# Performance work log

Measured on AMD Instinct MI355X. Metric: run time of the kernel, lower is better.

The kernel has to match this reference:

```python
import jax, jax.numpy as jnp
import numpy as np

NHEAD = 8
DIM_HEAD = 64
SCALE = DIM_HEAD ** (-0.5)


def setup_inputs() -> dict:
    key = jax.random.key(0)
    k1, k2, k3 = jax.random.split(key, 3)
    B, C, X, Y = 16, 256, 64, 64
    x = jax.random.normal(k1, (B, C, X, Y), dtype=jnp.float32)
    # 1x1 conv weights, represented as [out_channels, in_channels]
    w_qkv = jax.random.normal(k2, (3 * NHEAD * DIM_HEAD, C), dtype=jnp.float32) * (C ** -0.5)
    w_out = jax.random.normal(k3, (C, NHEAD * DIM_HEAD), dtype=jnp.float32) * ((NHEAD * DIM_HEAD) ** -0.5)
    return {"x": x, "w_qkv": w_qkv, "w_out": w_out}


def reference(x, w_qkv, w_out):
    B, C, X, Y = x.shape
    h, d = NHEAD, DIM_HEAD
    n = X * Y
    # 1x1 conv == channel-wise matmul
    qkv = jnp.einsum('bcxy,oc->boxy', x, w_qkv)          # [B, 3*h*d, X, Y]
    qkv = qkv.reshape(B, 3, h, d, n)                     # chunk along channels then (h c)
    q, k, v = qkv[:, 0], qkv[:, 1], qkv[:, 2]            # each [B, h, d, n]
    q = jax.nn.softmax(q, axis=-2) * SCALE               # softmax over feature dim d
    k = jax.nn.softmax(k, axis=-1)                       # softmax over token dim n
    phi_kv = jnp.einsum('bhdn,bhen->bhde', k, v)         # [B, h, d, d]
    att = jnp.einsum('bhde,bhdn->bhen', phi_kv, q)       # [B, h, d, n]
    att = att.reshape(B, h * d, X, Y)
    out = jnp.einsum('bexy,ce->bcxy', att, w_out)        # [B, C, X, Y]
    return out
```

## Files before the change

kernel.cpp:

```cpp
#include <hip/hip_runtime.h>
#include <hip/hip_bf16.h>


typedef __attribute__((ext_vector_type(8))) short bf16x8;
typedef __attribute__((ext_vector_type(4))) float f32x4;

__device__ __forceinline__ unsigned short f2bf(float f) {
    union { float f; unsigned int i; } w; w.f = f;
    unsigned int r = w.i + 0x7FFFu + ((w.i >> 16) & 1u);
    return (unsigned short)(r >> 16);
}

__device__ __forceinline__ void gload16(const unsigned short* g, unsigned short* l) {
    __builtin_amdgcn_global_load_lds(
        (const __attribute__((address_space(1))) void*)(const void*)g,
        (__attribute__((address_space(3))) void*)(void*)l,
        16, 0, 0);
}

__global__ __launch_bounds__(256) void cvt_w_frag(
    const float* __restrict__ wqkv, unsigned short* __restrict__ wf)
{
    int g = blockIdx.x * 256 + threadIdx.x;
    int lane = g & 63;
    int ks   = (g >> 6) & 7;
    int w2   = (g >> 9) & 3;
    int h    = (g >> 11) & 7;
    int op   = g >> 14;
    int row = op * 512 + h * 64 + w2 * 16 + (lane & 15);
    int col = ks * 32 + (lane >> 4) * 8;
    const float* src = &wqkv[(size_t)row * 256 + col];
    float4 f0 = *(const float4*)&src[0];
    float4 f1 = *(const float4*)&src[4];
    unsigned short t[8] = {f2bf(f0.x), f2bf(f0.y), f2bf(f0.z), f2bf(f0.w),
                           f2bf(f1.x), f2bf(f1.y), f2bf(f1.z), f2bf(f1.w)};
    *(uint4*)&wf[(size_t)g * 8] = *(uint4*)t;
}

__global__ __launch_bounds__(256) void cvt_xT(
    const float* __restrict__ x, unsigned short* __restrict__ xT)
{
    const int nb = blockIdx.x * 64, cb = blockIdx.y * 64, b = blockIdx.z;
    __shared__ float Ts[64 * 65];
    const int tid = threadIdx.x;
    const int l = tid & 63, w = tid >> 6;
    const float* xb = x + ((size_t)b * 256 + cb) * 4096 + nb;
#pragma unroll
    for (int p = 0; p < 4; p++) {
        int c = p * 16 + (tid >> 4);
        int n4 = (tid & 15) * 4;
        float4 v = *(const float4*)&xb[(size_t)c * 4096 + n4];
        Ts[c * 65 + n4 + 0] = v.x; Ts[c * 65 + n4 + 1] = v.y;
        Ts[c * 65 + n4 + 2] = v.z; Ts[c * 65 + n4 + 3] = v.w;
    }
    __syncthreads();
    unsigned short t[16];
#pragma unroll
    for (int i = 0; i < 16; i++) t[i] = f2bf(Ts[(w * 16 + i) * 65 + l]);
    unsigned short* dst = xT + ((size_t)b * 4096 + nb + l) * 256 + cb + w * 16;
    *(uint4*)&dst[0] = *(uint4*)&t[0];
    *(uint4*)&dst[8] = *(uint4*)&t[8];
}

__global__ __launch_bounds__(256, 3) void q_gemm(
    const unsigned short* __restrict__ xT, const unsigned short* __restrict__ wf,
    unsigned short* __restrict__ qf)
{
    const int ch = blockIdx.x;
    const int h  = blockIdx.y;
    const int b  = blockIdx.z;
    const int tid  = threadIdx.x;
    const int lane = tid & 63;
    const int w    = tid >> 6;
    const int quad = lane >> 4;
    const int l15  = lane & 15;

    __shared__ unsigned short smem[16384];
    unsigned short* Bs = smem;
    float* red = (float*)smem;
    unsigned short* Qs = smem + 7168;

    const unsigned short* wfq = wf + ((size_t)((0 * 8 + h) * 4 + w) * 8) * 512 + lane * 8;
    bf16x8 aq[8];
#pragma unroll
    for (int i = 0; i < 8; i++) aq[i] = *(const bf16x8*)&wfq[i * 512];

    const int grow = lane >> 3;
    const int gch  = ((lane & 7) ^ grow) * 8;
    const int c0 = (quad ^ (l15 & 7)) * 8;
    const int c1 = ((quad + 4) ^ (l15 & 7)) * 8;

    for (int st = 0; st < 4; st++) {
        const int nb = ch * 512 + st * 128;
        const unsigned short* gbase =
            xT + ((size_t)b * 4096 + nb + w * 32 + grow) * 256 + gch;

        f32x4 accq[8];
#pragma unroll
        for (int i = 0; i < 8; i++) accq[i] = (f32x4)(0.f);

#pragma unroll
        for (int i = 0; i < 4; i++)
            gload16(gbase + i * 2048, Bs + w * 2048 + i * 512);
        __syncthreads();

#pragma unroll
        for (int ks = 0; ks < 4; ks++) {
            const int buf = ks & 1;
            if (ks < 3) {
                const unsigned short* gs = gbase + (ks + 1) * 64;
                unsigned short* ld = Bs + (buf ^ 1) * 8192 + w * 2048;
#pragma unroll
                for (int i = 0; i < 4; i++)
                    gload16(gs + i * 2048, ld + i * 512);
            }
            const unsigned short* bsr = Bs + buf * 8192 + l15 * 64;
#pragma unroll
            for (int nt = 0; nt < 8; nt++) {
                bf16x8 bv0 = *(const bf16x8*)&bsr[nt * 1024 + c0];
                bf16x8 bv1 = *(const bf16x8*)&bsr[nt * 1024 + c1];
                accq[nt] = __builtin_amdgcn_mfma_f32_16x16x32_bf16(aq[2 * ks], bv0, accq[nt], 0, 0, 0);
                accq[nt] = __builtin_amdgcn_mfma_f32_16x16x32_bf16(aq[2 * ks + 1], bv1, accq[nt], 0, 0, 0);
            }
            if (ks < 3) __syncthreads();
        }

#pragma unroll
        for (int nt = 0; nt < 8; nt++) {
#pragma unroll
            for (int r = 0; r < 4; r++) accq[nt][r] = __expf(accq[nt][r]);
            float s = accq[nt][0] + accq[nt][1] + accq[nt][2] + accq[nt][3];
            s += __shfl_xor(s, 16);
            s += __shfl_xor(s, 32);
            if (quad == 0) red[w * 128 + nt * 16 + l15] = s;
        }
        __syncthreads();
        if (tid < 128) {
            float t = red[tid] + red[128 + tid] + red[256 + tid] + red[384 + tid];
            red[512 + tid] = 0.125f / t;
        }
        __syncthreads();
#pragma unroll
        for (int nt = 0; nt < 8; nt++) {
            float li = red[512 + nt * 16 + l15];
            uint2 pp;
            pp.x = (unsigned int)f2bf(accq[nt][0] * li) |
                   ((unsigned int)f2bf(accq[nt][1] * li) << 16);
            pp.y = (unsigned int)f2bf(accq[nt][2] * li) |
                   ((unsigned int)f2bf(accq[nt][3] * li) << 16);
            *(uint2*)&Qs[(nt * 16 + l15) * 72 + w * 16 + quad * 4] = pp;
        }
        __syncthreads();
        {
            const int n = tid >> 1, half = tid & 1;
            const int nbIdx = ch * 4 + st;
            const int ksq = h * 2 + half;
            const size_t gbase2 =
                (((size_t)(b * 32 + nbIdx) * 16 + ksq) * 8 + (n >> 4)) * 64 + (n & 15);
#pragma unroll
            for (int u = 0; u < 4; u++)
                *(uint4*)&qf[(gbase2 + u * 16) * 8] = *(uint4*)&Qs[n * 72 + half * 32 + u * 8];
        }
        __syncthreads();
    }
}

__global__ __launch_bounds__(256, 2) void kv_phi(
    const unsigned short* __restrict__ xT, const unsigned short* __restrict__ wf,
    float* __restrict__ phi, float* __restrict__ lsum)
{
    const int ch = blockIdx.x;
    const int h  = blockIdx.y;
    const int b  = blockIdx.z;
    const int tid  = threadIdx.x;
    const int lane = tid & 63;
    const int w    = tid >> 6;
    const int quad = lane >> 4;
    const int l15  = lane & 15;

    __shared__ unsigned short smem[16384];
    unsigned short* Es = smem;
    unsigned short* Vs = smem + 8192;
    unsigned short* Bs = smem;

    const unsigned short* wfk = wf + ((size_t)((1 * 8 + h) * 4 + w) * 8) * 512 + lane * 8;
    const unsigned short* wfv = wf + ((size_t)((2 * 8 + h) * 4 + w) * 8) * 512 + lane * 8;

    f32x4 pacc[4];
#pragma unroll
    for (int i = 0; i < 4; i++) pacc[i] = (f32x4)(0.f);
    float lacc[4] = {0.f, 0.f, 0.f, 0.f};

    const int grow = lane >> 3;
    const int gch  = ((lane & 7) ^ grow) * 8;
    const int c0 = (quad ^ (l15 & 7)) * 8;
    const int c1 = ((quad + 4) ^ (l15 & 7)) * 8;

    for (int st = 0; st < 4; st++) {
        const int nb = ch * 512 + st * 128;
        const unsigned short* gbase =
            xT + ((size_t)b * 4096 + nb + w * 32 + grow) * 256 + gch;

        f32x4 acck[8], accv[8];
#pragma unroll
        for (int i = 0; i < 8; i++) {
            acck[i] = (f32x4)(0.f); accv[i] = (f32x4)(0.f);
        }

        __syncthreads();
#pragma unroll
        for (int i = 0; i < 4; i++)
            gload16(gbase + i * 2048, Bs + w * 2048 + i * 512);
        __syncthreads();

#pragma unroll
        for (int ks = 0; ks < 4; ks++) {
            const int buf = ks & 1;
            if (ks < 3) {
                const unsigned short* gs = gbase + (ks + 1) * 64;
                unsigned short* ld = Bs + (buf ^ 1) * 8192 + w * 2048;
#pragma unroll
                for (int i = 0; i < 4; i++)
                    gload16(gs + i * 2048, ld + i * 512);
            }
            bf16x8 ak0 = *(const bf16x8*)&wfk[(2 * ks) * 512];
            bf16x8 ak1 = *(const bf16x8*)&wfk[(2 * ks + 1) * 512];
            bf16x8 av0 = *(const bf16x8*)&wfv[(2 * ks) * 512];
            bf16x8 av1 = *(const bf16x8*)&wfv[(2 * ks + 1) * 512];
            const unsigned short* bsr = Bs + buf * 8192 + l15 * 64;
#pragma unroll
            for (int nt = 0; nt < 8; nt++) {
                bf16x8 bv0 = *(const bf16x8*)&bsr[nt * 1024 + c0];
                bf16x8 bv1 = *(const bf16x8*)&bsr[nt * 1024 + c1];
                acck[nt] = __builtin_amdgcn_mfma_f32_16x16x32_bf16(ak0, bv0, acck[nt], 0, 0, 0);
                accv[nt] = __builtin_amdgcn_mfma_f32_16x16x32_bf16(av0, bv0, accv[nt], 0, 0, 0);
                acck[nt] = __builtin_amdgcn_mfma_f32_16x16x32_bf16(ak1, bv1, acck[nt], 0, 0, 0);
                accv[nt] = __builtin_amdgcn_mfma_f32_16x16x32_bf16(av1, bv1, accv[nt], 0, 0, 0);
            }
            if (ks < 3) __syncthreads();
        }
        __syncthreads();

#pragma unroll
        for (int r = 0; r < 4; r++) {
            const int dl = quad * 4 + r;
            const int dbase = (w * 16 + dl) * 256 + (l15 & 7) * 2;
#pragma unroll
            for (int nt = 0; nt < 8; nt++) {
                const int pos = (2 * nt + (l15 >> 3)) ^ dl;
                float ek = __expf(acck[nt][r]);
                lacc[r] += ek;
                *(unsigned short*)((char*)Es + dbase + pos * 16) = f2bf(ek);
                *(unsigned short*)((char*)Vs + dbase + pos * 16) = f2bf(accv[nt][r]);
            }
        }
        __syncthreads();

#pragma unroll
        for (int k2 = 0; k2 < 4; k2++) {
            bf16x8 ae = *(bf16x8*)((char*)Es + (w * 16 + l15) * 256 +
                                   (((k2 * 4 + quad) ^ l15) * 16));
#pragma unroll
            for (int et = 0; et < 4; et++) {
                bf16x8 bv = *(bf16x8*)((char*)Vs + (et * 16 + l15) * 256 +
                                       (((k2 * 4 + quad) ^ l15) * 16));
                pacc[et] = __builtin_amdgcn_mfma_f32_16x16x32_bf16(ae, bv, pacc[et], 0, 0, 0);
            }
        }
    }

#pragma unroll
    for (int r = 0; r < 4; r++) {
        float s = lacc[r];
        s += __shfl_xor(s, 1); s += __shfl_xor(s, 2);
        s += __shfl_xor(s, 4); s += __shfl_xor(s, 8);
        if (l15 == 0)
            atomicAdd(&lsum[((size_t)b * 8 + h) * 64 + w * 16 + quad * 4 + r], s);
    }
    float* pp = phi + ((size_t)b * 8 + h) * 4096;
#pragma unroll
    for (int et = 0; et < 4; et++)
#pragma unroll
        for (int r = 0; r < 4; r++)
            atomicAdd(&pp[(w * 16 + quad * 4 + r) * 64 + et * 16 + l15], pacc[et][r]);
}

__global__ __launch_bounds__(256) void build_M(
    const float* __restrict__ phi, const float* __restrict__ lsum,
    const float* __restrict__ w_out, unsigned short* __restrict__ Mf)
{
    const int h = blockIdx.x, b = blockIdx.y;
    __shared__ float pT[64][68];
    const float* pp = phi + ((size_t)b * 8 + h) * 4096;
    const int tid = threadIdx.x;
    const int row = tid >> 2, ls = tid & 3;
#pragma unroll
    for (int u = 0; u < 4; u++) {
        int e0 = (ls + u * 4) * 4;
        float4 v = *(const float4*)&pp[row * 64 + e0];
        pT[e0 + 0][row] = v.x; pT[e0 + 1][row] = v.y;
        pT[e0 + 2][row] = v.z; pT[e0 + 3][row] = v.w;
    }
    __syncthreads();
    const int c = tid;
    float acc[64];
#pragma unroll
    for (int d = 0; d < 64; d++) acc[d] = 0.f;
    for (int e4 = 0; e4 < 16; e4++) {
        float4 wv = *(const float4*)&w_out[(size_t)c * 512 + h * 64 + e4 * 4];
        float wq[4] = {wv.x, wv.y, wv.z, wv.w};
#pragma unroll
        for (int qq = 0; qq < 4; qq++) {
            int e = e4 * 4 + qq;
#pragma unroll
            for (int d4 = 0; d4 < 16; d4++) {
                float4 p = *(const float4*)&pT[e][d4 * 4];
                acc[d4 * 4 + 0] += wq[qq] * p.x;
                acc[d4 * 4 + 1] += wq[qq] * p.y;
                acc[d4 * 4 + 2] += wq[qq] * p.z;
                acc[d4 * 4 + 3] += wq[qq] * p.w;
            }
        }
    }
    const float* lrow = lsum + ((size_t)b * 8 + h) * 64;
    unsigned short tmp[64];
#pragma unroll
    for (int d = 0; d < 64; d++) tmp[d] = f2bf(acc[d] / lrow[d]);
    const int ct = c >> 7, wr = (c >> 6) & 1, mi = (c >> 4) & 3, l15c = c & 15;
#pragma unroll
    for (int u = 0; u < 8; u++) {
        const int ksA = h * 2 + (u >> 2);
        const int quadA = u & 3;
        size_t gidx = ((((size_t)(b * 2 + ct) * 2 + wr) * 4 + mi) * 16 + ksA) * 64
                      + quadA * 16 + l15c;
        *(uint4*)&Mf[gidx * 8] = *(uint4*)&tmp[u * 8];
    }
}

__global__ __launch_bounds__(256, 3) void out_mfma(
    const unsigned short* __restrict__ Mf, const unsigned short* __restrict__ qf,
    float* __restrict__ out)
{
    const int nbIdx = blockIdx.x;
    const int ct    = blockIdx.y;
    const int b     = blockIdx.z;
    const int tid  = threadIdx.x;
    const int lane = tid & 63;
    const int w    = tid >> 6;
    const int wr   = w >> 1, wc = w & 1;
    const int quad = lane >> 4;
    const int l15  = lane & 15;

    f32x4 acc[4][4];
#pragma unroll
    for (int i = 0; i < 4; i++)
#pragma unroll
        for (int j = 0; j < 4; j++) acc[i][j] = (f32x4)(0.f);

    const unsigned short* Ab =
        Mf + ((((size_t)(b * 2 + ct) * 2 + wr) * 4) * 16) * 512 + lane * 8;
    const unsigned short* Bb =
        qf + (((size_t)(b * 32 + nbIdx) * 16) * 8) * 512 + lane * 8;

    for (int ks = 0; ks < 16; ks++) {
        bf16x8 af[4], bv[4];
#pragma unroll
        for (int mi = 0; mi < 4; mi++)
            af[mi] = *(const bf16x8*)&Ab[(size_t)(mi * 16 + ks) * 512];
#pragma unroll
        for (int ni = 0; ni < 4; ni++)
            bv[ni] = *(const bf16x8*)&Bb[(size_t)(ks * 8 + wc * 4 + ni) * 512];
#pragma unroll
        for (int mi = 0; mi < 4; mi++)
#pragma unroll
            for (int ni = 0; ni < 4; ni++)
                acc[mi][ni] = __builtin_amdgcn_mfma_f32_16x16x32_bf16(
                    af[mi], bv[ni], acc[mi][ni], 0, 0, 0);
    }
    float* ob = out + ((size_t)b * 256 + ct * 128 + wr * 64) * 4096
                + nbIdx * 128 + wc * 64;
#pragma unroll
    for (int mi = 0; mi < 4; mi++)
#pragma unroll
        for (int ni = 0; ni < 4; ni++)
#pragma unroll
            for (int r = 0; r < 4; r++)
                ob[(size_t)(mi * 16 + quad * 4 + r) * 4096 + ni * 16 + l15]
                    = acc[mi][ni][r];
}

extern "C" void kernel_launch(void* const* d_in, const int* in_sizes, int n_in,
                              void* d_out, int out_size, void* d_ws, size_t ws_size,
                              hipStream_t stream) {
    const float* x     = (const float*)d_in[0];
    const float* w_qkv = (const float*)d_in[1];
    const float* w_out = (const float*)d_in[2];
    float* out = (float*)d_out;

    char* ws = (char*)d_ws;
    unsigned short* qf = (unsigned short*)ws;
    unsigned short* wf = (unsigned short*)(ws + 67108864);
    float* lsum = (float*)(ws + 67895296);
    float* phi  = (float*)(ws + 67928064);
    unsigned short* Mf = (unsigned short*)(ws + 70025216);
    unsigned short* xT = (unsigned short*)(ws + 74219520);

    hipMemsetAsync(lsum, 0, (8192 + 524288) * sizeof(float), stream);

    cvt_w_frag<<<192, 256, 0, stream>>>(w_qkv, wf);
    cvt_xT<<<dim3(64, 4, 16), 256, 0, stream>>>(x, xT);
    q_gemm<<<dim3(8, 8, 16), 256, 0, stream>>>(xT, wf, qf);
    kv_phi<<<dim3(8, 8, 16), 256, 0, stream>>>(xT, wf, phi, lsum);
    build_M<<<dim3(8, 16), 256, 0, stream>>>(phi, lsum, w_out, Mf);
    out_mfma<<<dim3(32, 2, 16), 256, 0, stream>>>(Mf, qf, out);
}
```

Before: 262.9 us.

## Repartition kv_phi wave work by token rows instead of head-dim rows

Each wave in kv_phi now computes all 64 k/v feature rows for its own 32-token slice, instead of 16 feature rows across all 128 tokens. Each wave reads only its slice of the LDS activation tile and loads four weight fragments per k-step from global memory. This cuts LDS read traffic for the x tile but raises per-wave weight loads and register use for the fragment arrays and the 4x4 partial log-sum accumulators. The scatter into the exp/value staging buffers and the lsum atomics are re-indexed to match the new partition.

```diff
diff --git a/kernel.cpp b/kernel.cpp
--- a/kernel.cpp
+++ b/kernel.cpp
@@ -183,13 +183,17 @@
     unsigned short* Vs = smem + 8192;
     unsigned short* Bs = smem;
 
-    const unsigned short* wfk = wf + ((size_t)((1 * 8 + h) * 4 + w) * 8) * 512 + lane * 8;
-    const unsigned short* wfv = wf + ((size_t)((2 * 8 + h) * 4 + w) * 8) * 512 + lane * 8;
+    const unsigned short* wfkb = wf + ((size_t)(1 * 8 + h) * 4) * 8 * 512 + lane * 8;
+    const unsigned short* wfvb = wf + ((size_t)(2 * 8 + h) * 4) * 8 * 512 + lane * 8;
 
     f32x4 pacc[4];
 #pragma unroll
     for (int i = 0; i < 4; i++) pacc[i] = (f32x4)(0.f);
-    float lacc[4] = {0.f, 0.f, 0.f, 0.f};
+    float lacc[4][4];
+#pragma unroll
+    for (int i = 0; i < 4; i++)
+#pragma unroll
+        for (int j = 0; j < 4; j++) lacc[i][j] = 0.f;
 
     const int grow = lane >> 3;
     const int gch  = ((lane & 7) ^ grow) * 8;
@@ -201,11 +205,13 @@
         const unsigned short* gbase =
             xT + ((size_t)b * 4096 + nb + w * 32 + grow) * 256 + gch;
 
-        f32x4 acck[8], accv[8];
-#pragma unroll
-        for (int i = 0; i < 8; i++) {
-            acck[i] = (f32x4)(0.f); accv[i] = (f32x4)(0.f);
-        }
+        f32x4 acck[2][4], accv[2][4];
+#pragma unroll
+        for (int i = 0; i < 2; i++)
+#pragma unroll
+            for (int j = 0; j < 4; j++) {
+                acck[i][j] = (f32x4)(0.f); accv[i][j] = (f32x4)(0.f);
+            }
 
         __syncthreads();
 #pragma unroll
@@ -223,19 +229,26 @@
                 for (int i = 0; i < 4; i++)
                     gload16(gs + i * 2048, ld + i * 512);
             }
-            bf16x8 ak0 = *(const bf16x8*)&wfk[(2 * ks) * 512];
-            bf16x8 ak1 = *(const bf16x8*)&wfk[(2 * ks + 1) * 512];
-            bf16x8 av0 = *(const bf16x8*)&wfv[(2 * ks) * 512];
-            bf16x8 av1 = *(const bf16x8*)&wfv[(2 * ks + 1) * 512];
-            const unsigned short* bsr = Bs + buf * 8192 + l15 * 64;
-#pragma unroll
-            for (int nt = 0; nt < 8; nt++) {
-                bf16x8 bv0 = *(const bf16x8*)&bsr[nt * 1024 + c0];
-                bf16x8 bv1 = *(const bf16x8*)&bsr[nt * 1024 + c1];
-                acck[nt] = __builtin_amdgcn_mfma_f32_16x16x32_bf16(ak0, bv0, acck[nt], 0, 0, 0);
-                accv[nt] = __builtin_amdgcn_mfma_f32_16x16x32_bf16(av0, bv0, accv[nt], 0, 0, 0);
-                acck[nt] = __builtin_amdgcn_mfma_f32_16x16x32_bf16(ak1, bv1, acck[nt], 0, 0, 0);
-                accv[nt] = __builtin_amdgcn_mfma_f32_16x16x32_bf16(av1, bv1, accv[nt], 0, 0, 0);
+            const unsigned short* bsr = Bs + buf * 8192 + (w * 32 + l15) * 64;
+#pragma unroll
+            for (int s = 0; s < 2; s++) {
+                const int ks2 = 2 * ks + s;
+                const int cs = s ? c1 : c0;
+                bf16x8 ak[4], av[4];
+#pragma unroll
+                for (int dt = 0; dt < 4; dt++) {
+                    ak[dt] = *(const bf16x8*)&wfkb[(size_t)(dt * 8 + ks2) * 512];
+                    av[dt] = *(const bf16x8*)&wfvb[(size_t)(dt * 8 + ks2) * 512];
+                }
+                bf16x8 bv0 = *(const bf16x8*)&bsr[0 * 1024 + cs];
+                bf16x8 bv1 = *(const bf16x8*)&bsr[1 * 1024 + cs];
+#pragma unroll
+                for (int dt = 0; dt < 4; dt++) {
+                    acck[0][dt] = __builtin_amdgcn_mfma_f32_16x16x32_bf16(ak[dt], bv0, acck[0][dt], 0, 0, 0);
+                    accv[0][dt] = __builtin_amdgcn_mfma_f32_16x16x32_bf16(av[dt], bv0, accv[0][dt], 0, 0, 0);
+                    acck[1][dt] = __builtin_amdgcn_mfma_f32_16x16x32_bf16(ak[dt], bv1, acck[1][dt], 0, 0, 0);
+                    accv[1][dt] = __builtin_amdgcn_mfma_f32_16x16x32_bf16(av[dt], bv1, accv[1][dt], 0, 0, 0);
+                }
             }
             if (ks < 3) __syncthreads();
         }
@@ -244,14 +257,17 @@
 #pragma unroll
         for (int r = 0; r < 4; r++) {
             const int dl = quad * 4 + r;
-            const int dbase = (w * 16 + dl) * 256 + (l15 & 7) * 2;
-#pragma unroll
-            for (int nt = 0; nt < 8; nt++) {
-                const int pos = (2 * nt + (l15 >> 3)) ^ dl;
-                float ek = __expf(acck[nt][r]);
-                lacc[r] += ek;
-                *(unsigned short*)((char*)Es + dbase + pos * 16) = f2bf(ek);
-                *(unsigned short*)((char*)Vs + dbase + pos * 16) = f2bf(accv[nt][r]);
+#pragma unroll
+            for (int dt = 0; dt < 4; dt++) {
+                const int dbase = (dt * 16 + dl) * 256 + (l15 & 7) * 2;
+#pragma unroll
+                for (int nt = 0; nt < 2; nt++) {
+                    const int pos = (w * 4 + nt * 2 + (l15 >> 3)) ^ dl;
+                    float ek = __expf(acck[nt][dt][r]);
+                    lacc[dt][r] += ek;
+                    *(unsigned short*)((char*)Es + dbase + pos * 16) = f2bf(ek);
+                    *(unsigned short*)((char*)Vs + dbase + pos * 16) = f2bf(accv[nt][dt][r]);
+                }
             }
         }
         __syncthreads();
@@ -270,13 +286,15 @@
     }
 
 #pragma unroll
-    for (int r = 0; r < 4; r++) {
-        float s = lacc[r];
-        s += __shfl_xor(s, 1); s += __shfl_xor(s, 2);
-        s += __shfl_xor(s, 4); s += __shfl_xor(s, 8);
-        if (l15 == 0)
-            atomicAdd(&lsum[((size_t)b * 8 + h) * 64 + w * 16 + quad * 4 + r], s);
-    }
+    for (int dt = 0; dt < 4; dt++)
+#pragma unroll
+        for (int r = 0; r < 4; r++) {
+            float s = lacc[dt][r];
+            s += __shfl_xor(s, 1); s += __shfl_xor(s, 2);
+            s += __shfl_xor(s, 4); s += __shfl_xor(s, 8);
+            if (l15 == 0)
+                atomicAdd(&lsum[((size_t)b * 8 + h) * 64 + dt * 16 + quad * 4 + r], s);
+        }
     float* pp = phi + ((size_t)b * 8 + h) * 4096;
 #pragma unroll
     for (int et = 0; et < 4; et++)
```

After: 391.7 us. +49.0%, slower.
